# Kernel tuning notes

Measured on AMD Instinct MI355X. Metric: run time of the kernel, lower is better.

Reference implementation:

```python
import jax
import jax.numpy as jnp
from jax import lax
import numpy as np

N_PRE = 1024
N_POST = 2048
SEQ_LEN = 4096
DECAY = 0.9   # leak factor per timestep
V_TH = 1.0    # firing threshold


def setup_inputs() -> dict:
    key = jax.random.key(0)
    k1, k2 = jax.random.split(key)
    stim = (jax.random.uniform(k1, (N_PRE, SEQ_LEN), dtype=jnp.float32) < 0.1).astype(jnp.float32)  # sparse input spikes
    weights = jax.random.normal(k2, (N_POST, N_PRE), dtype=jnp.float32) * 0.05
    return {"stim": stim, "weights": weights}


def reference(stim, weights):
    # Synaptic currents for all timesteps at once: cal_post_input(stim[:, i]) == weights @ stim[:, i]
    currents = jnp.einsum("np,pt->nt", weights, stim)  # [n_post, T]

    def lif_step(v, i_t):
        # leaky integrate
        v = v * DECAY + i_t
        # fire
        s = (v >= V_TH).astype(v.dtype)
        # reset to 0 where spiked
        v_next = jnp.where(s > 0, jnp.zeros_like(v), v)
        return v_next, (s, v_next)

    v0 = jnp.zeros((N_POST,), dtype=stim.dtype)
    _, (spikes_t, v_t) = lax.scan(lif_step, v0, currents.T)  # scanned over T
    # transpose back to [n_post, T] to match spike_times / v buffers
    return spikes_t.T, v_t.T
```

## Files before the change

### kernel.cpp

```cpp
#include <hip/hip_runtime.h>

#define N_PRE 1024
#define N_POST 2048
#define SEQ_LEN 4096

#define KSPLIT 512

__device__ __forceinline__ float opaque(float x) {
  asm volatile("" : "+v"(x));
  return x;
}

__device__ __forceinline__ float load_dyn(const void* p, size_t idx, bool isbf) {
  if (isbf) {
    const unsigned short b = ((const unsigned short*)p)[idx];
    return __uint_as_float(((unsigned int)b) << 16);
  }
  return ((const float*)p)[idx];
}

__device__ __forceinline__ int sniff_flags(const void* W, const void* S, int tid,
                                           int* flags_sh) {
  if (tid < 64) {
    const unsigned short* uw = (const unsigned short*)W;
    const float f = fabsf(__uint_as_float(((unsigned int)uw[tid * 2]) << 16));
    const bool big = !(f < 64.f);
    const unsigned long long wb = __ballot(big);
    const unsigned short* us = (const unsigned short*)S;
    int hit = 0;
    for (int j = 0; j < 64; ++j) hit |= (us[tid * 128 + 2 * j] == 0x3F80u) ? 1 : 0;
    const unsigned long long sb = __ballot(hit != 0);
    if (tid == 0) *flags_sh = ((wb == 0ull) ? 1 : 0) | ((sb != 0ull) ? 2 : 0);
  }
  __syncthreads();
  return *flags_sh;
}

__global__ __launch_bounds__(256, 2) void snn_gemm_v2(const void* __restrict__ W,
                                                      const void* __restrict__ S,
                                                      float* __restrict__ C,
                                                      int t0, int chunkT) {
  __shared__ float As[16][132];
  __shared__ float Bs[16][132];
  __shared__ int flags_sh;
  const int tid = threadIdx.x;
  const int fl = sniff_flags(W, S, tid, &flags_sh);
  const bool w_bf = (fl & 1) != 0;
  const bool s_bf = (fl & 2) != 0;

  const int tx = tid & 15;
  const int ty = tid >> 4;
  const int m0 = blockIdx.y * 128;
  const int nl0 = blockIdx.x * 128;

  float acc0[8][8] = {{0.f}};
  float acc1[8][8] = {{0.f}};

  int k0 = 0;
#define KTILE_BODY(ACC)                                                          \
  {                                                                              \
                        \
    if (!w_bf) {                                                                 \
      const float* Wf = (const float*)W;                                         \
      const int row = tid >> 2;                                                  \
      const int c4 = (tid & 3) * 4;                                              \
      _Pragma("unroll") for (int h = 0; h < 2; ++h) {                            \
        const int m = row + 64 * h;                                              \
        const float4 va =                                                        \
            *(const float4*)&Wf[(size_t)(m0 + m) * N_PRE + k0 + c4];             \
        As[c4 + 0][m] = va.x; As[c4 + 1][m] = va.y;                              \
        As[c4 + 2][m] = va.z; As[c4 + 3][m] = va.w;                              \
      }                                                                          \
    } else {                                                                     \
      _Pragma("unroll") for (int e = 0; e < 8; ++e) {                            \
        const int idx = tid * 8 + e;                                             \
        const int m = idx >> 4, c = idx & 15;                                    \
        As[c][m] = load_dyn(W, (size_t)(m0 + m) * N_PRE + k0 + c, true);         \
      }                                                                          \
    }                                                                            \
                    \
    {                                                                            \
      const int r = tid >> 4;                                                    \
      const int c8 = (tid & 15) * 8;                                             \
      if (s_bf) {                                                                \
        const unsigned short* Sb = (const unsigned short*)S;                     \
        const uint4 u =                                                          \
            *(const uint4*)&Sb[(size_t)(k0 + r) * SEQ_LEN + t0 + nl0 + c8];      \
        Bs[r][c8 + 0] = __uint_as_float(u.x << 16);                              \
        Bs[r][c8 + 1] = __uint_as_float(u.x & 0xFFFF0000u);                      \
        Bs[r][c8 + 2] = __uint_as_float(u.y << 16);                              \
        Bs[r][c8 + 3] = __uint_as_float(u.y & 0xFFFF0000u);                      \
        Bs[r][c8 + 4] = __uint_as_float(u.z << 16);                              \
        Bs[r][c8 + 5] = __uint_as_float(u.z & 0xFFFF0000u);                      \
        Bs[r][c8 + 6] = __uint_as_float(u.w << 16);                              \
        Bs[r][c8 + 7] = __uint_as_float(u.w & 0xFFFF0000u);                      \
      } else {                                                                   \
        const float* Sf = (const float*)S;                                       \
        const size_t base = (size_t)(k0 + r) * SEQ_LEN + t0 + nl0 + c8;          \
        *(float4*)&Bs[r][c8] = *(const float4*)&Sf[base];                        \
        *(float4*)&Bs[r][c8 + 4] = *(const float4*)&Sf[base + 4];                \
      }                                                                          \
    }                                                                            \
    __syncthreads();                                                             \
    _Pragma("unroll") for (int k = 0; k < 16; ++k) {                             \
      float a[8], b[8];                                                          \
      *(float4*)&a[0] = *(const float4*)&As[k][ty * 8];                          \
      *(float4*)&a[4] = *(const float4*)&As[k][ty * 8 + 4];                      \
      *(float4*)&b[0] = *(const float4*)&Bs[k][tx * 8];                          \
      *(float4*)&b[4] = *(const float4*)&Bs[k][tx * 8 + 4];                      \
      _Pragma("unroll") for (int i = 0; i < 8; ++i)                              \
          _Pragma("unroll") for (int j = 0; j < 8; ++j)                          \
              ACC[i][j] += a[i] * b[j];       \
    }                                                                            \
    __syncthreads();                                                             \
  }

  for (; k0 < KSPLIT; k0 += 16) KTILE_BODY(acc0)
  for (; k0 < N_PRE; k0 += 16) KTILE_BODY(acc1)
#undef KTILE_BODY

#pragma unroll
  for (int i = 0; i < 8; ++i) {
    float r[8];
#pragma unroll
    for (int j = 0; j < 8; ++j) r[j] = acc0[i][j] + acc1[i][j];
    float* dst = &C[(size_t)(m0 + ty * 8 + i) * chunkT + nl0 + tx * 8];
    *(float4*)&dst[0] = make_float4(r[0], r[1], r[2], r[3]);
    *(float4*)&dst[4] = make_float4(r[4], r[5], r[6], r[7]);
  }
}

#define SROWS 16
#define STT 64
#define SPAD 68
__global__ __launch_bounds__(256) void snn_scan_v2(const float* __restrict__ cur,
                                                   float* __restrict__ spk,
                                                   float* __restrict__ vout,
                                                   float* __restrict__ v_carry,
                                                   int t0, int chunkT, int first) {
  __shared__ float c_t[2][SROWS][SPAD];
  __shared__ float s_t[SROWS][SPAD];
  __shared__ float v_t[SROWS][SPAD];
  const int tid = threadIdx.x;
  const int n0 = blockIdx.x * SROWS;
  const int row = tid >> 4;
  const int c4 = (tid & 15) * 4;

  float v = 0.0f;
  if (tid < SROWS && !first) v = v_carry[n0 + tid];

  const int ntiles = chunkT / STT;
  *(float4*)&c_t[0][row][c4] =
      *(const float4*)&cur[(size_t)(n0 + row) * chunkT + 0 + c4];
  __syncthreads();

  for (int it = 0; it < ntiles; ++it) {
    const int buf = it & 1;
    if (it + 1 < ntiles) {
      *(float4*)&c_t[buf ^ 1][row][c4] =
          *(const float4*)&cur[(size_t)(n0 + row) * chunkT + (it + 1) * STT + c4];
    }
    if (tid < SROWS) {
#pragma unroll
      for (int g = 0; g < STT / 16; ++g) {
        float c[16], s[16], vv[16];
        *(float4*)&c[0] = *(const float4*)&c_t[buf][tid][g * 16];
        *(float4*)&c[4] = *(const float4*)&c_t[buf][tid][g * 16 + 4];
        *(float4*)&c[8] = *(const float4*)&c_t[buf][tid][g * 16 + 8];
        *(float4*)&c[12] = *(const float4*)&c_t[buf][tid][g * 16 + 12];
#pragma unroll
        for (int k = 0; k < 16; ++k) {
          const float leak = opaque(v * 0.9f);
          v = leak + c[k];
          const bool fired = (v >= 1.0f);
          s[k] = fired ? 1.0f : 0.0f;
          v = fired ? 0.0f : v;
          vv[k] = v;
        }
        *(float4*)&s_t[tid][g * 16] = make_float4(s[0], s[1], s[2], s[3]);
        *(float4*)&s_t[tid][g * 16 + 4] = make_float4(s[4], s[5], s[6], s[7]);
        *(float4*)&s_t[tid][g * 16 + 8] = make_float4(s[8], s[9], s[10], s[11]);
        *(float4*)&s_t[tid][g * 16 + 12] = make_float4(s[12], s[13], s[14], s[15]);
        *(float4*)&v_t[tid][g * 16] = make_float4(vv[0], vv[1], vv[2], vv[3]);
        *(float4*)&v_t[tid][g * 16 + 4] = make_float4(vv[4], vv[5], vv[6], vv[7]);
        *(float4*)&v_t[tid][g * 16 + 8] = make_float4(vv[8], vv[9], vv[10], vv[11]);
        *(float4*)&v_t[tid][g * 16 + 12] = make_float4(vv[12], vv[13], vv[14], vv[15]);
      }
    }
    __syncthreads();
    {
      const size_t g = (size_t)(n0 + row) * SEQ_LEN + t0 + it * STT + c4;
      *(float4*)&spk[g] = *(const float4*)&s_t[row][c4];
      *(float4*)&vout[g] = *(const float4*)&v_t[row][c4];
    }
    __syncthreads();
  }

  if (tid < SROWS) v_carry[n0 + tid] = v;
}

__global__ __launch_bounds__(256) void snn_fused_blis(const void* __restrict__ W,
                                                      const void* __restrict__ S,
                                                      float* __restrict__ spk,
                                                      float* __restrict__ vout) {
  __shared__ float As[16][68];
  __shared__ float Bs[16][68];
  __shared__ float Ct[64][65];
  __shared__ float vsh[64];
  __shared__ int flags_sh;
  const int tid = threadIdx.x;
  const int fl = sniff_flags(W, S, tid, &flags_sh);
  const bool w_bf = (fl & 1) != 0;
  const bool s_bf = (fl & 2) != 0;

  const int tx = tid & 15;
  const int ty = tid >> 4;
  const int m0 = blockIdx.x * 64;
  if (tid < 64) vsh[tid] = 0.0f;

  for (int t0 = 0; t0 < SEQ_LEN; t0 += 64) {
    float acc0[4][4] = {{0.f}};
    float acc1[4][4] = {{0.f}};
    int k0 = 0;
#define FUSED_SEGMENT(ACC, KEND)                                                 \
    for (; k0 < (KEND); k0 += 16) {                                              \
      {                                                                          \
        const int r = tid >> 4, c = tid & 15;                                    \
        _Pragma("unroll") for (int j = 0; j < 4; ++j)                            \
            As[c][r + 16 * j] =                                                  \
                load_dyn(W, (size_t)(m0 + r + 16 * j) * N_PRE + k0 + c, w_bf);   \
      }                                                                          \
      {                                                                          \
        const int r = tid >> 6, c = tid & 63;                                    \
        _Pragma("unroll") for (int j = 0; j < 4; ++j)                            \
            Bs[r + 4 * j][c] =                                                   \
                load_dyn(S, (size_t)(k0 + r + 4 * j) * SEQ_LEN + t0 + c, s_bf);  \
      }                                                                          \
      __syncthreads();                                                           \
      _Pragma("unroll") for (int k = 0; k < 16; ++k) {                           \
        _Pragma("unroll") for (int i = 0; i < 4; ++i)                            \
            _Pragma("unroll") for (int j = 0; j < 4; ++j)                        \
                ACC[i][j] += As[k][ty * 4 + i] * Bs[k][tx * 4 + j];              \
      }                                                                          \
      __syncthreads();                                                           \
    }

    FUSED_SEGMENT(acc0, KSPLIT)
    FUSED_SEGMENT(acc1, N_PRE)
#undef FUSED_SEGMENT

#pragma unroll
    for (int i = 0; i < 4; ++i)
#pragma unroll
      for (int j = 0; j < 4; ++j) Ct[ty * 4 + i][tx * 4 + j] = acc0[i][j] + acc1[i][j];
    __syncthreads();
    if (tid < 64) {
      float v = vsh[tid];
#pragma unroll
      for (int k = 0; k < 64; ++k) {
        const float leak = opaque(v * 0.9f);
        v = leak + Ct[tid][k];
        const bool fired = (v >= 1.0f);
        const size_t g = (size_t)(m0 + tid) * SEQ_LEN + t0 + k;
        spk[g] = fired ? 1.0f : 0.0f;
        v = fired ? 0.0f : v;
        vout[g] = v;
      }
      vsh[tid] = v;
    }
    __syncthreads();
  }
}

extern "C" void kernel_launch(void* const* d_in, const int* in_sizes, int n_in,
                              void* d_out, int out_size, void* d_ws, size_t ws_size,
                              hipStream_t stream) {
  const void* stim = d_in[0];
  const void* weights = d_in[1];
  if (n_in >= 2 && in_sizes[0] == N_POST * N_PRE && in_sizes[1] == N_PRE * SEQ_LEN) {
    weights = d_in[0];
    stim = d_in[1];
  }

  float* spk = (float*)d_out;
  float* vout = spk + (size_t)N_POST * SEQ_LEN;

  const size_t carry_bytes = (size_t)N_POST * sizeof(float);
  float* v_carry = nullptr;
  size_t avail = 0;
  if (ws_size > carry_bytes + 8) {
    const size_t coff = (ws_size - carry_bytes) & ~(size_t)15;
    v_carry = (float*)((char*)d_ws + coff);
    avail = coff;
  }
  int chunkT = (int)((avail / ((size_t)N_POST * sizeof(float))) / 128 * 128);
  if (chunkT > SEQ_LEN) chunkT = SEQ_LEN;

  if (chunkT >= 128) {
    float* cur = (float*)d_ws;
    for (int t0 = 0; t0 < SEQ_LEN; t0 += chunkT) {
      const int ct = (SEQ_LEN - t0 < chunkT) ? (SEQ_LEN - t0) : chunkT;
      snn_gemm_v2<<<dim3(ct / 128, N_POST / 128), dim3(256), 0, stream>>>(weights, stim, cur,
                                                                          t0, ct);
      snn_scan_v2<<<dim3(N_POST / SROWS), dim3(256), 0, stream>>>(cur, spk, vout, v_carry,
                                                                  t0, ct, t0 == 0);
    }
  } else {
    snn_fused_blis<<<dim3(N_POST / 64), dim3(256), 0, stream>>>(weights, stim, spk, vout);
  }
}
```

Measured before the change: 415.8 us.

## Split GEMM over K across grid, shrink tiles, and slim scan kernel

```diff
diff --git a/kernel.cpp b/kernel.cpp
--- a/kernel.cpp
+++ b/kernel.cpp
@@ -36,138 +36,145 @@
   return *flags_sh;
 }
 
-__global__ __launch_bounds__(256, 2) void snn_gemm_v2(const void* __restrict__ W,
+__global__ __launch_bounds__(128, 4) void snn_gemm_v3(const void* __restrict__ W,
                                                       const void* __restrict__ S,
                                                       float* __restrict__ C,
-                                                      int t0, int chunkT) {
+                                                      int t0, int ct) {
   __shared__ float As[16][132];
-  __shared__ float Bs[16][132];
+  __shared__ float Bs[16][68];
   __shared__ int flags_sh;
   const int tid = threadIdx.x;
   const int fl = sniff_flags(W, S, tid, &flags_sh);
   const bool w_bf = (fl & 1) != 0;
   const bool s_bf = (fl & 2) != 0;
 
-  const int tx = tid & 15;
-  const int ty = tid >> 4;
+  const int tx = tid & 7;
+  const int ty = tid >> 3;
   const int m0 = blockIdx.y * 128;
-  const int nl0 = blockIdx.x * 128;
-
-  float acc0[8][8] = {{0.f}};
-  float acc1[8][8] = {{0.f}};
-
-  int k0 = 0;
-#define KTILE_BODY(ACC)                                                          \
-  {                                                                              \
-                        \
-    if (!w_bf) {                                                                 \
-      const float* Wf = (const float*)W;                                         \
-      const int row = tid >> 2;                                                  \
-      const int c4 = (tid & 3) * 4;                                              \
-      _Pragma("unroll") for (int h = 0; h < 2; ++h) {                            \
-        const int m = row + 64 * h;                                              \
-        const float4 va =                                                        \
-            *(const float4*)&Wf[(size_t)(m0 + m) * N_PRE + k0 + c4];             \
-        As[c4 + 0][m] = va.x; As[c4 + 1][m] = va.y;                              \
-        As[c4 + 2][m] = va.z; As[c4 + 3][m] = va.w;                              \
-      }                                                                          \
-    } else {                                                                     \
-      _Pragma("unroll") for (int e = 0; e < 8; ++e) {                            \
-        const int idx = tid * 8 + e;                                             \
-        const int m = idx >> 4, c = idx & 15;                                    \
-        As[c][m] = load_dyn(W, (size_t)(m0 + m) * N_PRE + k0 + c, true);         \
-      }                                                                          \
-    }                                                                            \
-                    \
-    {                                                                            \
-      const int r = tid >> 4;                                                    \
-      const int c8 = (tid & 15) * 8;                                             \
-      if (s_bf) {                                                                \
-        const unsigned short* Sb = (const unsigned short*)S;                     \
-        const uint4 u =                                                          \
-            *(const uint4*)&Sb[(size_t)(k0 + r) * SEQ_LEN + t0 + nl0 + c8];      \
-        Bs[r][c8 + 0] = __uint_as_float(u.x << 16);                              \
-        Bs[r][c8 + 1] = __uint_as_float(u.x & 0xFFFF0000u);                      \
-        Bs[r][c8 + 2] = __uint_as_float(u.y << 16);                              \
-        Bs[r][c8 + 3] = __uint_as_float(u.y & 0xFFFF0000u);                      \
-        Bs[r][c8 + 4] = __uint_as_float(u.z << 16);                              \
-        Bs[r][c8 + 5] = __uint_as_float(u.z & 0xFFFF0000u);                      \
-        Bs[r][c8 + 6] = __uint_as_float(u.w << 16);                              \
-        Bs[r][c8 + 7] = __uint_as_float(u.w & 0xFFFF0000u);                      \
-      } else {                                                                   \
-        const float* Sf = (const float*)S;                                       \
-        const size_t base = (size_t)(k0 + r) * SEQ_LEN + t0 + nl0 + c8;          \
-        *(float4*)&Bs[r][c8] = *(const float4*)&Sf[base];                        \
-        *(float4*)&Bs[r][c8 + 4] = *(const float4*)&Sf[base + 4];                \
-      }                                                                          \
-    }                                                                            \
-    __syncthreads();                                                             \
-    _Pragma("unroll") for (int k = 0; k < 16; ++k) {                             \
-      float a[8], b[8];                                                          \
-      *(float4*)&a[0] = *(const float4*)&As[k][ty * 8];                          \
-      *(float4*)&a[4] = *(const float4*)&As[k][ty * 8 + 4];                      \
-      *(float4*)&b[0] = *(const float4*)&Bs[k][tx * 8];                          \
-      *(float4*)&b[4] = *(const float4*)&Bs[k][tx * 8 + 4];                      \
-      _Pragma("unroll") for (int i = 0; i < 8; ++i)                              \
-          _Pragma("unroll") for (int j = 0; j < 8; ++j)                          \
-              ACC[i][j] += a[i] * b[j];       \
-    }                                                                            \
-    __syncthreads();                                                             \
-  }
-
-  for (; k0 < KSPLIT; k0 += 16) KTILE_BODY(acc0)
-  for (; k0 < N_PRE; k0 += 16) KTILE_BODY(acc1)
-#undef KTILE_BODY
-
+  const int nl0 = blockIdx.x * 64;
+  const int kbeg = (int)blockIdx.z * KSPLIT;
+
+  float acc[8][8] = {{0.f}};
+
+  for (int k0 = kbeg; k0 < kbeg + KSPLIT; k0 += 16) {
+    if (!w_bf) {
+      const float* Wf = (const float*)W;
+      const int c4 = (tid & 3) * 4;
+      const int mr = tid >> 2;
+#pragma unroll
+      for (int h = 0; h < 4; ++h) {
+        const int m = mr + 32 * h;
+        const float4 va = *(const float4*)&Wf[(size_t)(m0 + m) * N_PRE + k0 + c4];
+        As[c4 + 0][m] = va.x; As[c4 + 1][m] = va.y;
+        As[c4 + 2][m] = va.z; As[c4 + 3][m] = va.w;
+      }
+    } else {
+#pragma unroll
+      for (int e = 0; e < 16; ++e) {
+        const int idx = tid * 16 + e;
+        const int m = idx >> 4, c = idx & 15;
+        As[c][m] = load_dyn(W, (size_t)(m0 + m) * N_PRE + k0 + c, true);
+      }
+    }
+    {
+      const int r = tid >> 3;
+      const int c8 = (tid & 7) * 8;
+      if (s_bf) {
+        const unsigned short* Sb = (const unsigned short*)S;
+        const uint4 u =
+            *(const uint4*)&Sb[(size_t)(k0 + r) * SEQ_LEN + t0 + nl0 + c8];
+        *(float4*)&Bs[r][c8] = make_float4(
+            __uint_as_float(u.x << 16), __uint_as_float(u.x & 0xFFFF0000u),
+            __uint_as_float(u.y << 16), __uint_as_float(u.y & 0xFFFF0000u));
+        *(float4*)&Bs[r][c8 + 4] = make_float4(
+            __uint_as_float(u.z << 16), __uint_as_float(u.z & 0xFFFF0000u),
+            __uint_as_float(u.w << 16), __uint_as_float(u.w & 0xFFFF0000u));
+      } else {
+        const float* Sf = (const float*)S;
+        const size_t base = (size_t)(k0 + r) * SEQ_LEN + t0 + nl0 + c8;
+        *(float4*)&Bs[r][c8] = *(const float4*)&Sf[base];
+        *(float4*)&Bs[r][c8 + 4] = *(const float4*)&Sf[base + 4];
+      }
+    }
+    __syncthreads();
+#pragma unroll
+    for (int k = 0; k < 16; ++k) {
+      float a[8], b[8];
+      *(float4*)&a[0] = *(const float4*)&As[k][ty * 8];
+      *(float4*)&a[4] = *(const float4*)&As[k][ty * 8 + 4];
+      *(float4*)&b[0] = *(const float4*)&Bs[k][tx * 8];
+      *(float4*)&b[4] = *(const float4*)&Bs[k][tx * 8 + 4];
+#pragma unroll
+      for (int i = 0; i < 8; ++i)
+#pragma unroll
+        for (int j = 0; j < 8; ++j)
+          acc[i][j] += a[i] * b[j];
+    }
+    __syncthreads();
+  }
+
+  float* Cseg = C + (size_t)blockIdx.z * N_POST * (size_t)ct;
 #pragma unroll
   for (int i = 0; i < 8; ++i) {
-    float r[8];
-#pragma unroll
-    for (int j = 0; j < 8; ++j) r[j] = acc0[i][j] + acc1[i][j];
-    float* dst = &C[(size_t)(m0 + ty * 8 + i) * chunkT + nl0 + tx * 8];
-    *(float4*)&dst[0] = make_float4(r[0], r[1], r[2], r[3]);
-    *(float4*)&dst[4] = make_float4(r[4], r[5], r[6], r[7]);
-  }
-}
-
-#define SROWS 16
-#define STT 64
-#define SPAD 68
-__global__ __launch_bounds__(256) void snn_scan_v2(const float* __restrict__ cur,
-                                                   float* __restrict__ spk,
-                                                   float* __restrict__ vout,
-                                                   float* __restrict__ v_carry,
-                                                   int t0, int chunkT, int first) {
-  __shared__ float c_t[2][SROWS][SPAD];
-  __shared__ float s_t[SROWS][SPAD];
-  __shared__ float v_t[SROWS][SPAD];
-  const int tid = threadIdx.x;
-  const int n0 = blockIdx.x * SROWS;
-  const int row = tid >> 4;
-  const int c4 = (tid & 15) * 4;
+    float* dst = &Cseg[(size_t)(m0 + ty * 8 + i) * ct + nl0 + tx * 8];
+    *(float4*)&dst[0] = make_float4(acc[i][0], acc[i][1], acc[i][2], acc[i][3]);
+    *(float4*)&dst[4] = make_float4(acc[i][4], acc[i][5], acc[i][6], acc[i][7]);
+  }
+}
+
+#define SCAN_R 8
+#define SCAN_T 64
+#define SCAN_P 68
+__global__ __launch_bounds__(64) void snn_scan_v3(const float* __restrict__ C,
+                                                  float* __restrict__ spk,
+                                                  float* __restrict__ vout,
+                                                  float* __restrict__ v_carry,
+                                                  int t0, int ct, int first) {
+  __shared__ float c_t[2][SCAN_R][SCAN_P];
+  const int l = threadIdx.x;
+  const int n0 = blockIdx.x * SCAN_R;
+  const float* C1 = C + (size_t)N_POST * (size_t)ct;
 
   float v = 0.0f;
-  if (tid < SROWS && !first) v = v_carry[n0 + tid];
-
-  const int ntiles = chunkT / STT;
-  *(float4*)&c_t[0][row][c4] =
-      *(const float4*)&cur[(size_t)(n0 + row) * chunkT + 0 + c4];
-  __syncthreads();
-
+  if (l < SCAN_R && !first) v = v_carry[n0 + l];
+
+  const int r0 = l >> 4;
+  const int c4 = (l & 15) * 4;
+  const int ntiles = ct / SCAN_T;
+
+#pragma unroll
+  for (int h = 0; h < 2; ++h) {
+    const int r = r0 + 4 * h;
+    const size_t g = (size_t)(n0 + r) * ct + c4;
+    const float4 a = *(const float4*)&C[g];
+    const float4 b = *(const float4*)&C1[g];
+    *(float4*)&c_t[0][r][c4] =
+        make_float4(a.x + b.x, a.y + b.y, a.z + b.z, a.w + b.w);
+  }
+
+  int buf = 0;
   for (int it = 0; it < ntiles; ++it) {
-    const int buf = it & 1;
-    if (it + 1 < ntiles) {
-      *(float4*)&c_t[buf ^ 1][row][c4] =
-          *(const float4*)&cur[(size_t)(n0 + row) * chunkT + (it + 1) * STT + c4];
-    }
-    if (tid < SROWS) {
-#pragma unroll
-      for (int g = 0; g < STT / 16; ++g) {
-        float c[16], s[16], vv[16];
-        *(float4*)&c[0] = *(const float4*)&c_t[buf][tid][g * 16];
-        *(float4*)&c[4] = *(const float4*)&c_t[buf][tid][g * 16 + 4];
-        *(float4*)&c[8] = *(const float4*)&c_t[buf][tid][g * 16 + 8];
-        *(float4*)&c[12] = *(const float4*)&c_t[buf][tid][g * 16 + 12];
+    float4 pa[2], pb[2];
+    const bool pf = (it + 1 < ntiles);
+    if (pf) {
+#pragma unroll
+      for (int h = 0; h < 2; ++h) {
+        const int r = r0 + 4 * h;
+        const size_t g = (size_t)(n0 + r) * ct + (size_t)(it + 1) * SCAN_T + c4;
+        pa[h] = *(const float4*)&C[g];
+        pb[h] = *(const float4*)&C1[g];
+      }
+    }
+    if (l < SCAN_R) {
+      const size_t gout = (size_t)(n0 + l) * SEQ_LEN + t0 + (size_t)it * SCAN_T;
+#pragma unroll
+      for (int g = 0; g < SCAN_T / 16; ++g) {
+        float c[16];
+        *(float4*)&c[0] = *(const float4*)&c_t[buf][l][g * 16];
+        *(float4*)&c[4] = *(const float4*)&c_t[buf][l][g * 16 + 4];
+        *(float4*)&c[8] = *(const float4*)&c_t[buf][l][g * 16 + 8];
+        *(float4*)&c[12] = *(const float4*)&c_t[buf][l][g * 16 + 12];
+        float s[16], vv[16];
 #pragma unroll
         for (int k = 0; k < 16; ++k) {
           const float leak = opaque(v * 0.9f);
@@ -177,26 +184,27 @@
           v = fired ? 0.0f : v;
           vv[k] = v;
         }
-        *(float4*)&s_t[tid][g * 16] = make_float4(s[0], s[1], s[2], s[3]);
-        *(float4*)&s_t[tid][g * 16 + 4] = make_float4(s[4], s[5], s[6], s[7]);
-        *(float4*)&s_t[tid][g * 16 + 8] = make_float4(s[8], s[9], s[10], s[11]);
-        *(float4*)&s_t[tid][g * 16 + 12] = make_float4(s[12], s[13], s[14], s[15]);
-        *(float4*)&v_t[tid][g * 16] = make_float4(vv[0], vv[1], vv[2], vv[3]);
-        *(float4*)&v_t[tid][g * 16 + 4] = make_float4(vv[4], vv[5], vv[6], vv[7]);
-        *(float4*)&v_t[tid][g * 16 + 8] = make_float4(vv[8], vv[9], vv[10], vv[11]);
-        *(float4*)&v_t[tid][g * 16 + 12] = make_float4(vv[12], vv[13], vv[14], vv[15]);
-      }
-    }
-    __syncthreads();
-    {
-      const size_t g = (size_t)(n0 + row) * SEQ_LEN + t0 + it * STT + c4;
-      *(float4*)&spk[g] = *(const float4*)&s_t[row][c4];
-      *(float4*)&vout[g] = *(const float4*)&v_t[row][c4];
-    }
-    __syncthreads();
-  }
-
-  if (tid < SROWS) v_carry[n0 + tid] = v;
+#pragma unroll
+        for (int q = 0; q < 4; ++q) {
+          *(float4*)&spk[gout + g * 16 + q * 4] =
+              make_float4(s[q * 4], s[q * 4 + 1], s[q * 4 + 2], s[q * 4 + 3]);
+          *(float4*)&vout[gout + g * 16 + q * 4] =
+              make_float4(vv[q * 4], vv[q * 4 + 1], vv[q * 4 + 2], vv[q * 4 + 3]);
+        }
+      }
+    }
+    if (pf) {
+#pragma unroll
+      for (int h = 0; h < 2; ++h) {
+        const int r = r0 + 4 * h;
+        *(float4*)&c_t[buf ^ 1][r][c4] =
+            make_float4(pa[h].x + pb[h].x, pa[h].y + pb[h].y, pa[h].z + pb[h].z,
+                        pa[h].w + pb[h].w);
+      }
+    }
+    buf ^= 1;
+  }
+  if (l < SCAN_R) v_carry[n0 + l] = v;
 }
 
 __global__ __launch_bounds__(256) void snn_fused_blis(const void* __restrict__ W,
@@ -293,17 +301,17 @@
     v_carry = (float*)((char*)d_ws + coff);
     avail = coff;
   }
-  int chunkT = (int)((avail / ((size_t)N_POST * sizeof(float))) / 128 * 128);
+  int chunkT = (int)((avail / ((size_t)N_POST * sizeof(float) * 2)) / 64 * 64);
   if (chunkT > SEQ_LEN) chunkT = SEQ_LEN;
 
-  if (chunkT >= 128) {
+  if (chunkT >= 64) {
     float* cur = (float*)d_ws;
     for (int t0 = 0; t0 < SEQ_LEN; t0 += chunkT) {
       const int ct = (SEQ_LEN - t0 < chunkT) ? (SEQ_LEN - t0) : chunkT;
-      snn_gemm_v2<<<dim3(ct / 128, N_POST / 128), dim3(256), 0, stream>>>(weights, stim, cur,
-                                                                          t0, ct);
-      snn_scan_v2<<<dim3(N_POST / SROWS), dim3(256), 0, stream>>>(cur, spk, vout, v_carry,
-                                                                  t0, ct, t0 == 0);
+      snn_gemm_v3<<<dim3(ct / 64, N_POST / 128, 2), dim3(128), 0, stream>>>(
+          weights, stim, cur, t0, ct);
+      snn_scan_v3<<<dim3(N_POST / SCAN_R), dim3(64), 0, stream>>>(
+          cur, spk, vout, v_carry, t0, ct, t0 == 0);
     }
   } else {
     snn_fused_blis<<<dim3(N_POST / 64), dim3(256), 0, stream>>>(weights, stim, spk, vout);
```

Measured after the change: 1.315 ms. 3.16x slower.
